# Optimization experiments

Measured on AMD Instinct MI355X. Metric: run time of the kernel, lower is better.

The kernel has to match this reference:

```python
import jax, jax.numpy as jnp
import numpy as np

Q_HEADS = 16
KV_HEADS = 4
ROPE_THETA = 10000.0


def _rope(x, seq_len):
    # x: [B, S, H, D]; pairs are consecutive along D (view_as_complex semantics)
    D = x.shape[-1]
    inv_freq = 1.0 / (ROPE_THETA ** (jnp.arange(0, D, 2, dtype=jnp.float32) / D))
    freqs = jnp.arange(seq_len, dtype=jnp.float32)[:, None] * inv_freq  # [S, D/2]
    cos = jnp.cos(freqs)[None, :, None, :]
    sin = jnp.sin(freqs)[None, :, None, :]
    xr = x.reshape(x.shape[:-1] + (D // 2, 2))
    x0, x1 = xr[..., 0], xr[..., 1]
    out = jnp.stack([x0 * cos - x1 * sin, x0 * sin + x1 * cos], axis=-1)
    return out.reshape(x.shape)


def setup_inputs() -> dict:
    key = jax.random.key(0)
    ks = jax.random.split(key, 6)
    B, S, E = 1, 2048, 2048
    KV_DIM = KV_HEADS * (E // Q_HEADS)  # 512
    scale = 0.02
    return {
        "x": jax.random.normal(ks[0], (B, S, E), dtype=jnp.float32),
        "Wq": jax.random.normal(ks[1], (E, E), dtype=jnp.float32) * scale,
        "Wk": jax.random.normal(ks[2], (KV_DIM, E), dtype=jnp.float32) * scale,
        "Wv": jax.random.normal(ks[3], (KV_DIM, E), dtype=jnp.float32) * scale,
        "Wo": jax.random.normal(ks[4], (E, E), dtype=jnp.float32) * scale,
        "bo": jax.random.normal(ks[5], (E,), dtype=jnp.float32) * scale,
        "cache_keys": jnp.zeros((B, S, KV_HEADS, E // Q_HEADS), dtype=jnp.float32),
        "cache_value": jnp.zeros((B, S, KV_HEADS, E // Q_HEADS), dtype=jnp.float32),
        "start_pos": 0,
    }


def reference(x, Wq, Wk, Wv, Wo, bo, cache_keys, cache_value, start_pos):
    B, S, E = x.shape
    hd = E // Q_HEADS
    G = Q_HEADS // KV_HEADS  # queries per kv head

    xq = (x @ Wq.T).reshape(B, S, Q_HEADS, hd)
    xk = (x @ Wk.T).reshape(B, S, KV_HEADS, hd)
    xv = (x @ Wv.T).reshape(B, S, KV_HEADS, hd)

    # Original applies RoPE with positions 0..seq_len-1 for both q and k
    # (freq tensor is sliced [:seq_len] inside apply_rotry_position_embedding).
    xq = _rope(xq, S)
    xk = _rope(xk, S)

    # cache write at start_pos (static python int)
    cache_keys = jax.lax.dynamic_update_slice(cache_keys, xk, (0, start_pos, 0, 0))
    cache_value = jax.lax.dynamic_update_slice(cache_value, xv, (0, start_pos, 0, 0))
    total = start_pos + S
    k_full = cache_keys[:, :total]   # [B, T, KVH, hd]
    v_full = cache_value[:, :total]

    # repeat_interleave over the head axis == GQA expansion
    k = jnp.repeat(k_full, G, axis=2)  # [B, T, QH, hd]
    v = jnp.repeat(v_full, G, axis=2)

    scores = jnp.einsum("bshd,bthd->bhst", xq, k) / jnp.sqrt(jnp.float32(hd))
    causal = jnp.triu(jnp.ones((S, total), dtype=bool), k=1)  # [S, T]
    scores = jnp.where(causal[None, None, :, :], -jnp.inf, scores)
    weights = jax.nn.softmax(scores, axis=-1)
    out = jnp.einsum("bhst,bthd->bshd", weights, v).reshape(B, S, E)
    # dropout p=0.0 / eval mode -> identity
    return out @ Wo.T + bo
```

## Files before the change

kernel.cpp:

```cpp
#include <hip/hip_runtime.h>
#include <stdint.h>

typedef unsigned short u16;
typedef float  f32x4  __attribute__((ext_vector_type(4)));
typedef __bf16 bf16x8 __attribute__((ext_vector_type(8)));
typedef __bf16 bf16x4 __attribute__((ext_vector_type(4)));
typedef unsigned short u16x8 __attribute__((ext_vector_type(8)));
typedef unsigned short u16x4v __attribute__((ext_vector_type(4)));

#define S_LEN 2048
#define E_DIM 2048
#define HD    128
#define QH    16
#define KVH   4
#define KVD   512
#define NQKV  3072
#define QK_SCALE 0.08838834764831845f

#define AS1 __attribute__((address_space(1)))
#define AS3 __attribute__((address_space(3)))

__device__ __forceinline__ u16 f2bf(float f) {
  union { float f; uint32_t u; } v; v.f = f;
  return (u16)((v.u + 0x7FFFu + ((v.u >> 16) & 1u)) >> 16);
}
__device__ __forceinline__ float bf2f(u16 b) {
  union { uint32_t u; float f; } v; v.u = ((uint32_t)b) << 16;
  return v.f;
}

__global__ void cast_all_kernel(const float* __restrict__ x, const float* __restrict__ Wq,
                                const float* __restrict__ Wk, const float* __restrict__ Wv,
                                const float* __restrict__ Wo,
                                u16* __restrict__ xb, u16* __restrict__ Wcat,
                                u16* __restrict__ Wob) {
  int i = blockIdx.x * blockDim.x + threadIdx.x;
  const float* src; u16* dst;
  if (i < (1 << 20))                       { src = x  + (size_t)i * 4;  dst = xb + (size_t)i * 4; }
  else if (i < (2 << 20))                  { size_t j = i - (1 << 20);  src = Wq + j * 4; dst = Wcat + j * 4; }
  else if (i < (2 << 20) + (1 << 18))      { size_t j = i - (2 << 20);  src = Wk + j * 4; dst = Wcat + (size_t)E_DIM * E_DIM + j * 4; }
  else if (i < (2 << 20) + (2 << 18))      { size_t j = i - (2 << 20) - (1 << 18); src = Wv + j * 4; dst = Wcat + (size_t)(E_DIM + KVD) * E_DIM + j * 4; }
  else                                     { size_t j = i - (2 << 20) - (2 << 18); src = Wo + j * 4; dst = Wob + j * 4; }
  float4 f = *reinterpret_cast<const float4*>(src);
  u16x4v o;
  o[0] = f2bf(f.x); o[1] = f2bf(f.y); o[2] = f2bf(f.z); o[3] = f2bf(f.w);
  *reinterpret_cast<u16x4v*>(dst) = o;
}

template<bool BIAS, bool OBF16>
__global__ __launch_bounds__(512) void gemm_bt_kernel(
    const u16* __restrict__ A, const u16* __restrict__ B,
    void* __restrict__ Cv, const float* __restrict__ bias,
    int M, int N, int K)
{
  __shared__ u16 As[2][128 * 64];
  __shared__ u16 Bs[2][128 * 64];

  const int tid  = threadIdx.x;
  const int lane = tid & 63;
  const int wid  = tid >> 6;
  const int wr   = (wid >> 2) * 64;
  const int wc   = (wid & 3) * 32;
  const int lr   = lane & 15;
  const int kg   = lane >> 4;
  const int sw   = lr & 7;

  const int bm = blockIdx.y * 128;
  const int bn = blockIdx.x * 128;

  f32x4 acc[4][2];
  #pragma unroll
  for (int r = 0; r < 4; ++r)
    #pragma unroll
    for (int c = 0; c < 2; ++c) acc[r][c] = (f32x4){0.f, 0.f, 0.f, 0.f};

  const int srow   = wid * 8 + (lane >> 3);
  const int schunk = (lane & 7) ^ (lane >> 3);

  const u16* gA = A + (size_t)(bm + srow) * K + schunk * 8;
  const u16* gB = B + (size_t)(bn + srow) * K + schunk * 8;

  auto stage = [&](int buf, int kt) {
    #pragma unroll
    for (int i = 0; i < 2; ++i) {
      __builtin_amdgcn_global_load_lds(
          (const AS1 void*)(gA + (size_t)i * 64 * K + kt),
          (AS3 void*)(&As[buf][(wid*8 + i*64) * 64]), 16, 0, 0);
      __builtin_amdgcn_global_load_lds(
          (const AS1 void*)(gB + (size_t)i * 64 * K + kt),
          (AS3 void*)(&Bs[buf][(wid*8 + i*64) * 64]), 16, 0, 0);
    }
  };

  stage(0, 0);
  __syncthreads();

  int cur = 0;
  for (int kt = 0; kt < K; kt += 64) {
    if (kt + 64 < K) stage(cur ^ 1, kt + 64);
    #pragma unroll
    for (int kk = 0; kk < 2; ++kk) {
      bf16x8 af[4], bfr[2];
      #pragma unroll
      for (int r = 0; r < 4; ++r)
        af[r] = *reinterpret_cast<const bf16x8*>(
            &As[cur][(wr + r*16 + lr)*64 + ((kk*4 + kg) ^ sw)*8]);
      #pragma unroll
      for (int c = 0; c < 2; ++c)
        bfr[c] = *reinterpret_cast<const bf16x8*>(
            &Bs[cur][(wc + c*16 + lr)*64 + ((kk*4 + kg) ^ sw)*8]);
      #pragma unroll
      for (int r = 0; r < 4; ++r)
        #pragma unroll
        for (int c = 0; c < 2; ++c)
          acc[r][c] = __builtin_amdgcn_mfma_f32_16x16x32_bf16(af[r], bfr[c], acc[r][c], 0, 0, 0);
    }
    __syncthreads();
    cur ^= 1;
  }

  const int crow = kg * 4;
  #pragma unroll
  for (int r = 0; r < 4; ++r) {
    #pragma unroll
    for (int c = 0; c < 2; ++c) {
      int gr = bm + wr + r*16 + crow;
      int gc = bn + wc + c*16 + lr;
      float badd = BIAS ? bias[gc] : 0.0f;
      #pragma unroll
      for (int reg = 0; reg < 4; ++reg) {
        float v = acc[r][c][reg] + badd;
        if constexpr (OBF16)
          ((u16*)Cv)[(size_t)(gr + reg)*N + gc] = f2bf(v);
        else
          ((float*)Cv)[(size_t)(gr + reg)*N + gc] = v;
      }
    }
  }
}

__global__ void rope_split_kernel(const u16* __restrict__ qkv,
                                  u16* __restrict__ qb, u16* __restrict__ kb) {
  int idx = blockIdx.x * blockDim.x + threadIdx.x;
  int s  = idx / 1280;
  int cp = idx - s * 1280;
  int col = cp * 2;
  const u16* src = qkv + (size_t)s * NQKV + col;
  float x0 = bf2f(src[0]), x1 = bf2f(src[1]);
  int p = (col & 127) >> 1;
  float inv = exp2f((float)p * (-13.287712379549449f / 64.0f));
  float ang = (float)s * inv;
  float sn, cs;
  sincosf(ang, &sn, &cs);
  float o0 = x0 * cs - x1 * sn;
  float o1 = x0 * sn + x1 * cs;
  if (col < E_DIM) {
    o0 *= QK_SCALE; o1 *= QK_SCALE;
    qb[(size_t)s * E_DIM + col]     = f2bf(o0);
    qb[(size_t)s * E_DIM + col + 1] = f2bf(o1);
  } else {
    kb[(size_t)s * KVD + (col - E_DIM)]     = f2bf(o0);
    kb[(size_t)s * KVD + (col - E_DIM) + 1] = f2bf(o1);
  }
}

__global__ void transpose_v_kernel(const u16* __restrict__ qkv, u16* __restrict__ vT) {
  __shared__ u16 tile[32][33];
  const int sbase = blockIdx.x * 32;
  const int cbase = blockIdx.y * 32;
  const int tx = threadIdx.x;
  const int ty = threadIdx.y;
  #pragma unroll
  for (int i = 0; i < 32; i += 8)
    tile[ty + i][tx] = qkv[(size_t)(sbase + ty + i) * NQKV + (E_DIM + KVD) + cbase + tx];
  __syncthreads();
  #pragma unroll
  for (int i = 0; i < 32; i += 8)
    vT[(size_t)(cbase + ty + i) * S_LEN + sbase + tx] = tile[tx][ty + i];
}

__device__ __forceinline__ void attn_tile(
    int t, int qt, int wid, int lr, int kg,
    const bf16x8* qf, f32x4* o, float& mr, float& ls,
    const u16* ks, const u16* vts, u16* ps)
{
  const int sw = lr & 7;
  f32x4 st[4];
  #pragma unroll
  for (int c = 0; c < 4; ++c) st[c] = (f32x4){0.f, 0.f, 0.f, 0.f};
  __builtin_amdgcn_s_setprio(1);
  #pragma unroll
  for (int kk = 0; kk < 4; ++kk) {
    #pragma unroll
    for (int c = 0; c < 4; ++c) {
      bf16x8 kfr = *reinterpret_cast<const bf16x8*>(
          &ks[(c*16 + lr)*128 + ((kk*4 + kg) ^ sw)*8]);
      st[c] = __builtin_amdgcn_mfma_f32_16x16x32_bf16(kfr, qf[kk], st[c], 0, 0, 0);
    }
  }
  __builtin_amdgcn_s_setprio(0);
  if (t == qt) {
    #pragma unroll
    for (int c = 0; c < 4; ++c)
      #pragma unroll
      for (int reg = 0; reg < 4; ++reg)
        if (c*16 + kg*4 + reg > wid*16 + lr) st[c][reg] = -1e30f;
  }
  float cm[4];
  #pragma unroll
  for (int c = 0; c < 4; ++c)
    cm[c] = fmaxf(fmaxf(st[c][0], st[c][1]), fmaxf(st[c][2], st[c][3]));
  float pm = fmaxf(fmaxf(cm[0], cm[1]), fmaxf(cm[2], cm[3]));
  pm = fmaxf(pm, __shfl_xor(pm, 16));
  pm = fmaxf(pm, __shfl_xor(pm, 32));

  if (!__all(pm - mr <= 8.0f)) {
    float nm = fmaxf(mr, pm);
    float alpha = __expf(mr - nm);
    ls *= alpha;
    mr = nm;
    float ar[4];
    #pragma unroll
    for (int reg = 0; reg < 4; ++reg)
      ar[reg] = __shfl(alpha, kg*4 + reg);
    #pragma unroll
    for (int d = 0; d < 8; ++d)
      #pragma unroll
      for (int reg = 0; reg < 4; ++reg)
        o[d][reg] *= ar[reg];
  }

  float p[4][4];
  float csum[4];
  #pragma unroll
  for (int c = 0; c < 4; ++c) {
    #pragma unroll
    for (int reg = 0; reg < 4; ++reg)
      p[c][reg] = __expf(st[c][reg] - mr);
    csum[c] = (p[c][0] + p[c][1]) + (p[c][2] + p[c][3]);
  }
  float sum = (csum[0] + csum[1]) + (csum[2] + csum[3]);
  sum += __shfl_xor(sum, 16);
  sum += __shfl_xor(sum, 32);
  ls += sum;

  #pragma unroll
  for (int c = 0; c < 4; ++c) {
    bf16x4 pk;
    #pragma unroll
    for (int reg = 0; reg < 4; ++reg) pk[reg] = (__bf16)p[c][reg];
    *reinterpret_cast<bf16x4*>(&ps[lr*72 + c*16 + kg*4]) = pk;
  }
  __builtin_amdgcn_s_setprio(1);
  #pragma unroll
  for (int kk = 0; kk < 2; ++kk) {
    bf16x8 pa = *reinterpret_cast<const bf16x8*>(&ps[lr*72 + kk*32 + kg*8]);
    #pragma unroll
    for (int d = 0; d < 8; ++d) {
      bf16x8 vb = *reinterpret_cast<const bf16x8*>(
          &vts[(d*16 + lr)*64 + ((kk*4 + kg) ^ sw)*8]);
      o[d] = __builtin_amdgcn_mfma_f32_16x16x32_bf16(pa, vb, o[d], 0, 0, 0);
    }
  }
  __builtin_amdgcn_s_setprio(0);
}

__global__ __launch_bounds__(256, 2) void attn_kernel(
    const u16* __restrict__ Q, const u16* __restrict__ Kc,
    const u16* __restrict__ VT, u16* __restrict__ Out)
{
  __shared__ u16 Ks[2][64 * 128];
  __shared__ u16 VTs[2][128 * 64];
  __shared__ u16 Ps[4][16 * 72];

  const int x = blockIdx.x;
  int qt, h;
  if (x < 256) { qt = x & 31; h = x >> 5; }
  else         { int xp = x - 256; qt = 31 - (xp & 31); h = 8 + (xp >> 5); }
  const int kvh = h >> 2;
  const int tid  = threadIdx.x;
  const int lane = tid & 63;
  const int wid  = tid >> 6;
  const int lr   = lane & 15;
  const int kg   = lane >> 4;

  const int NT = qt + 1;

  bf16x8 qf[4];
  {
    const u16* qa = Q + (size_t)(qt*64 + wid*16 + lr) * E_DIM + h * HD + kg * 8;
    #pragma unroll
    for (int kk = 0; kk < 4; ++kk)
      qf[kk] = *reinterpret_cast<const bf16x8*>(qa + kk * 32);
  }

  f32x4 o[8];
  #pragma unroll
  for (int d = 0; d < 8; ++d) o[d] = (f32x4){0.f,0.f,0.f,0.f};
  float mr = -1e30f, ls = 0.f;

  u16x8 kreg[4], vreg[4];
  const u16* kbase = Kc + kvh * HD;
  const u16* vbase = VT + (size_t)(kvh * HD) * S_LEN;

  auto stage_load = [&](int t) {
    #pragma unroll
    for (int i = 0; i < 4; ++i) {
      int c = i * 256 + tid;
      kreg[i] = *reinterpret_cast<const u16x8*>(
          kbase + (size_t)(t*64 + (c >> 4)) * KVD + (c & 15) * 8);
      vreg[i] = *reinterpret_cast<const u16x8*>(
          vbase + (size_t)(c >> 3) * S_LEN + t*64 + (c & 7) * 8);
    }
  };
  auto stage_write = [&](int b) {
    #pragma unroll
    for (int i = 0; i < 4; ++i) {
      int c = i * 256 + tid;
      int kr = c >> 4, kc = c & 15;
      *reinterpret_cast<u16x8*>(&Ks[b][kr*128 + (kc ^ (kr & 7))*8]) = kreg[i];
      int vr = c >> 3, vc = c & 7;
      *reinterpret_cast<u16x8*>(&VTs[b][vr*64 + (vc ^ (vr & 7))*8]) = vreg[i];
    }
  };

  int p = 0;
  stage_load(0);
  stage_write(0);
  __syncthreads();

  for (int t = 0; t < NT; ++t) {
    if (t + 1 < NT) stage_load(t + 1);
    attn_tile(t, qt, wid, lr, kg, qf, o, mr, ls, Ks[p], VTs[p], Ps[wid]);
    if (t + 1 < NT) {
      stage_write(p ^ 1);
      __syncthreads();
      p ^= 1;
    }
  }

  {
    float inv = 1.0f / ls;
    float ivq[4];
    #pragma unroll
    for (int reg = 0; reg < 4; ++reg)
      ivq[reg] = __shfl(inv, kg*4 + reg);
    #pragma unroll
    for (int reg = 0; reg < 4; ++reg) {
      int grow = qt*64 + wid*16 + kg*4 + reg;
      #pragma unroll
      for (int d = 0; d < 8; ++d)
        Out[(size_t)grow * E_DIM + h * HD + d*16 + lr] =
            __builtin_bit_cast(u16, (__bf16)(o[d][reg] * ivq[reg]));
    }
  }
}

extern "C" void kernel_launch(void* const* d_in, const int* in_sizes, int n_in,
                              void* d_out, int out_size, void* d_ws, size_t ws_size,
                              hipStream_t stream)
{
  const float* x  = (const float*)d_in[0];
  const float* Wq = (const float*)d_in[1];
  const float* Wk = (const float*)d_in[2];
  const float* Wv = (const float*)d_in[3];
  const float* Wo = (const float*)d_in[4];
  const float* bo = (const float*)d_in[5];
  float* out = (float*)d_out;

  char* w = (char*)d_ws;
  u16*   xb   = (u16*)(w);
  u16*   Wcat = (u16*)(w + (8u  << 20));
  u16*   Wob  = (u16*)(w + (20u << 20));
  u16*   qkv  = (u16*)(w + (28u << 20));
  u16*   qb   = (u16*)(w + (52u << 20));
  u16*   kb   = (u16*)(w + (60u << 20));
  u16*   vT   = (u16*)(w + (62u << 20));
  u16*   attn = (u16*)(w + (64u << 20));
  (void)ws_size; (void)in_sizes; (void)n_in; (void)out_size;

  cast_all_kernel<<<14336, 256, 0, stream>>>(x, Wq, Wk, Wv, Wo, xb, Wcat, Wob);

  gemm_bt_kernel<false, true><<<dim3(NQKV/128, S_LEN/128), 512, 0, stream>>>(
      xb, Wcat, qkv, nullptr, S_LEN, NQKV, E_DIM);

  rope_split_kernel<<<(S_LEN * 1280) / 256, 256, 0, stream>>>(qkv, qb, kb);
  transpose_v_kernel<<<dim3(S_LEN/32, KVD/32), dim3(32, 8), 0, stream>>>(qkv, vT);

  attn_kernel<<<512, 256, 0, stream>>>(qb, kb, vT, attn);

  gemm_bt_kernel<true, false><<<dim3(E_DIM/128, S_LEN/128), 512, 0, stream>>>(
      attn, Wob, out, bo, S_LEN, E_DIM, E_DIM);
}
```

Measured before the change: 139.9 us.

## Pair causal query tiles and share KV across two heads per attention block

Restructures attention so each block processes two heads sharing a KV head, and each wave handles 32 query rows, reusing K/V fragments across two MFMA streams. Each block runs two phases with complementary causal tiles (qt and 31-qt) to balance work, and the grid is reduced to 256 blocks with one block per CU. The grid indexing maps each complementary pair twice, so every output tile is computed redundantly, and the occupancy drop reduces latency hiding.

```diff
diff --git a/kernel.cpp b/kernel.cpp
--- a/kernel.cpp
+++ b/kernel.cpp
@@ -179,130 +179,35 @@
     vT[(size_t)(cbase + ty + i) * S_LEN + sbase + tx] = tile[tx][ty + i];
 }
 
-__device__ __forceinline__ void attn_tile(
-    int t, int qt, int wid, int lr, int kg,
-    const bf16x8* qf, f32x4* o, float& mr, float& ls,
-    const u16* ks, const u16* vts, u16* ps)
-{
-  const int sw = lr & 7;
-  f32x4 st[4];
-  #pragma unroll
-  for (int c = 0; c < 4; ++c) st[c] = (f32x4){0.f, 0.f, 0.f, 0.f};
-  __builtin_amdgcn_s_setprio(1);
-  #pragma unroll
-  for (int kk = 0; kk < 4; ++kk) {
-    #pragma unroll
-    for (int c = 0; c < 4; ++c) {
-      bf16x8 kfr = *reinterpret_cast<const bf16x8*>(
-          &ks[(c*16 + lr)*128 + ((kk*4 + kg) ^ sw)*8]);
-      st[c] = __builtin_amdgcn_mfma_f32_16x16x32_bf16(kfr, qf[kk], st[c], 0, 0, 0);
-    }
-  }
-  __builtin_amdgcn_s_setprio(0);
-  if (t == qt) {
-    #pragma unroll
-    for (int c = 0; c < 4; ++c)
-      #pragma unroll
-      for (int reg = 0; reg < 4; ++reg)
-        if (c*16 + kg*4 + reg > wid*16 + lr) st[c][reg] = -1e30f;
-  }
-  float cm[4];
-  #pragma unroll
-  for (int c = 0; c < 4; ++c)
-    cm[c] = fmaxf(fmaxf(st[c][0], st[c][1]), fmaxf(st[c][2], st[c][3]));
-  float pm = fmaxf(fmaxf(cm[0], cm[1]), fmaxf(cm[2], cm[3]));
-  pm = fmaxf(pm, __shfl_xor(pm, 16));
-  pm = fmaxf(pm, __shfl_xor(pm, 32));
-
-  if (!__all(pm - mr <= 8.0f)) {
-    float nm = fmaxf(mr, pm);
-    float alpha = __expf(mr - nm);
-    ls *= alpha;
-    mr = nm;
-    float ar[4];
-    #pragma unroll
-    for (int reg = 0; reg < 4; ++reg)
-      ar[reg] = __shfl(alpha, kg*4 + reg);
-    #pragma unroll
-    for (int d = 0; d < 8; ++d)
-      #pragma unroll
-      for (int reg = 0; reg < 4; ++reg)
-        o[d][reg] *= ar[reg];
-  }
-
-  float p[4][4];
-  float csum[4];
-  #pragma unroll
-  for (int c = 0; c < 4; ++c) {
-    #pragma unroll
-    for (int reg = 0; reg < 4; ++reg)
-      p[c][reg] = __expf(st[c][reg] - mr);
-    csum[c] = (p[c][0] + p[c][1]) + (p[c][2] + p[c][3]);
-  }
-  float sum = (csum[0] + csum[1]) + (csum[2] + csum[3]);
-  sum += __shfl_xor(sum, 16);
-  sum += __shfl_xor(sum, 32);
-  ls += sum;
-
-  #pragma unroll
-  for (int c = 0; c < 4; ++c) {
-    bf16x4 pk;
-    #pragma unroll
-    for (int reg = 0; reg < 4; ++reg) pk[reg] = (__bf16)p[c][reg];
-    *reinterpret_cast<bf16x4*>(&ps[lr*72 + c*16 + kg*4]) = pk;
-  }
-  __builtin_amdgcn_s_setprio(1);
-  #pragma unroll
-  for (int kk = 0; kk < 2; ++kk) {
-    bf16x8 pa = *reinterpret_cast<const bf16x8*>(&ps[lr*72 + kk*32 + kg*8]);
-    #pragma unroll
-    for (int d = 0; d < 8; ++d) {
-      bf16x8 vb = *reinterpret_cast<const bf16x8*>(
-          &vts[(d*16 + lr)*64 + ((kk*4 + kg) ^ sw)*8]);
-      o[d] = __builtin_amdgcn_mfma_f32_16x16x32_bf16(pa, vb, o[d], 0, 0, 0);
-    }
-  }
-  __builtin_amdgcn_s_setprio(0);
-}
-
-__global__ __launch_bounds__(256, 2) void attn_kernel(
+__global__ __launch_bounds__(256, 1) void attn_kernel(
     const u16* __restrict__ Q, const u16* __restrict__ Kc,
     const u16* __restrict__ VT, u16* __restrict__ Out)
 {
   __shared__ u16 Ks[2][64 * 128];
   __shared__ u16 VTs[2][128 * 64];
-  __shared__ u16 Ps[4][16 * 72];
-
-  const int x = blockIdx.x;
-  int qt, h;
-  if (x < 256) { qt = x & 31; h = x >> 5; }
-  else         { int xp = x - 256; qt = 31 - (xp & 31); h = 8 + (xp >> 5); }
-  const int kvh = h >> 2;
+  __shared__ u16 Ps[4][32 * 72];
+
+  const int x    = blockIdx.x;
+  const int hp   = x & 7;
+  const int qtA  = (x >> 3) & 31;
+  const int qtB  = 31 - qtA;
+  const int h0   = hp * 2;
+  const int kvh  = h0 >> 2;
+
   const int tid  = threadIdx.x;
   const int lane = tid & 63;
   const int wid  = tid >> 6;
+  const int head = h0 + (wid & 1);
+  const int rowbase = (wid >> 1) * 32;
   const int lr   = lane & 15;
   const int kg   = lane >> 4;
-
-  const int NT = qt + 1;
-
-  bf16x8 qf[4];
-  {
-    const u16* qa = Q + (size_t)(qt*64 + wid*16 + lr) * E_DIM + h * HD + kg * 8;
-    #pragma unroll
-    for (int kk = 0; kk < 4; ++kk)
-      qf[kk] = *reinterpret_cast<const bf16x8*>(qa + kk * 32);
-  }
-
-  f32x4 o[8];
-  #pragma unroll
-  for (int d = 0; d < 8; ++d) o[d] = (f32x4){0.f,0.f,0.f,0.f};
-  float mr = -1e30f, ls = 0.f;
-
-  u16x8 kreg[4], vreg[4];
+  const int sw   = lr & 7;
+
   const u16* kbase = Kc + kvh * HD;
   const u16* vbase = VT + (size_t)(kvh * HD) * S_LEN;
-
+  u16* ps = Ps[wid];
+
+  u16x8 kreg[4], vreg[4];
   auto stage_load = [&](int t) {
     #pragma unroll
     for (int i = 0; i < 4; ++i) {
@@ -324,36 +229,154 @@
     }
   };
 
-  int p = 0;
-  stage_load(0);
-  stage_write(0);
-  __syncthreads();
-
-  for (int t = 0; t < NT; ++t) {
-    if (t + 1 < NT) stage_load(t + 1);
-    attn_tile(t, qt, wid, lr, kg, qf, o, mr, ls, Ks[p], VTs[p], Ps[wid]);
-    if (t + 1 < NT) {
-      stage_write(p ^ 1);
-      __syncthreads();
-      p ^= 1;
-    }
-  }
-
-  {
-    float inv = 1.0f / ls;
-    float ivq[4];
-    #pragma unroll
-    for (int reg = 0; reg < 4; ++reg)
-      ivq[reg] = __shfl(inv, kg*4 + reg);
-    #pragma unroll
-    for (int reg = 0; reg < 4; ++reg) {
-      int grow = qt*64 + wid*16 + kg*4 + reg;
-      #pragma unroll
-      for (int d = 0; d < 8; ++d)
-        Out[(size_t)grow * E_DIM + h * HD + d*16 + lr] =
-            __builtin_bit_cast(u16, (__bf16)(o[d][reg] * ivq[reg]));
-    }
-  }
+  auto run_phase = [&](int qt) {
+    const int NT = qt + 1;
+
+    bf16x8 qf[2][4];
+    #pragma unroll
+    for (int g = 0; g < 2; ++g) {
+      const u16* qa = Q + (size_t)(qt*64 + rowbase + g*16 + lr) * E_DIM
+                        + head * HD + kg * 8;
+      #pragma unroll
+      for (int kk = 0; kk < 4; ++kk)
+        qf[g][kk] = *reinterpret_cast<const bf16x8*>(qa + kk * 32);
+    }
+
+    f32x4 o[2][8];
+    #pragma unroll
+    for (int g = 0; g < 2; ++g)
+      #pragma unroll
+      for (int d = 0; d < 8; ++d) o[g][d] = (f32x4){0.f,0.f,0.f,0.f};
+    float mr[2] = {-1e30f, -1e30f}, ls[2] = {0.f, 0.f};
+
+    stage_load(0);
+    __syncthreads();
+    stage_write(0);
+    __syncthreads();
+
+    int p = 0;
+    for (int t = 0; t < NT; ++t) {
+      if (t + 1 < NT) stage_load(t + 1);
+
+      f32x4 st[2][4];
+      #pragma unroll
+      for (int g = 0; g < 2; ++g)
+        #pragma unroll
+        for (int c = 0; c < 4; ++c) st[g][c] = (f32x4){0.f,0.f,0.f,0.f};
+      __builtin_amdgcn_s_setprio(1);
+      #pragma unroll
+      for (int kk = 0; kk < 4; ++kk) {
+        #pragma unroll
+        for (int c = 0; c < 4; ++c) {
+          bf16x8 kfr = *reinterpret_cast<const bf16x8*>(
+              &Ks[p][(c*16 + lr)*128 + ((kk*4 + kg) ^ sw)*8]);
+          st[0][c] = __builtin_amdgcn_mfma_f32_16x16x32_bf16(kfr, qf[0][kk], st[0][c], 0, 0, 0);
+          st[1][c] = __builtin_amdgcn_mfma_f32_16x16x32_bf16(kfr, qf[1][kk], st[1][c], 0, 0, 0);
+        }
+      }
+      __builtin_amdgcn_s_setprio(0);
+
+      if (t == qt) {
+        #pragma unroll
+        for (int g = 0; g < 2; ++g)
+          #pragma unroll
+          for (int c = 0; c < 4; ++c)
+            #pragma unroll
+            for (int reg = 0; reg < 4; ++reg)
+              if (c*16 + kg*4 + reg > rowbase + g*16 + lr) st[g][c][reg] = -1e30f;
+      }
+
+      #pragma unroll
+      for (int g = 0; g < 2; ++g) {
+        float cm[4];
+        #pragma unroll
+        for (int c = 0; c < 4; ++c)
+          cm[c] = fmaxf(fmaxf(st[g][c][0], st[g][c][1]), fmaxf(st[g][c][2], st[g][c][3]));
+        float pm = fmaxf(fmaxf(cm[0], cm[1]), fmaxf(cm[2], cm[3]));
+        pm = fmaxf(pm, __shfl_xor(pm, 16));
+        pm = fmaxf(pm, __shfl_xor(pm, 32));
+
+        if (!__all(pm - mr[g] <= 8.0f)) {
+          float nm = fmaxf(mr[g], pm);
+          float alpha = __expf(mr[g] - nm);
+          ls[g] *= alpha;
+          mr[g] = nm;
+          float ar[4];
+          #pragma unroll
+          for (int reg = 0; reg < 4; ++reg)
+            ar[reg] = __shfl(alpha, kg*4 + reg);
+          #pragma unroll
+          for (int d = 0; d < 8; ++d)
+            #pragma unroll
+            for (int reg = 0; reg < 4; ++reg)
+              o[g][d][reg] *= ar[reg];
+        }
+
+        float sum = 0.f;
+        #pragma unroll
+        for (int c = 0; c < 4; ++c) {
+          float pr[4];
+          #pragma unroll
+          for (int reg = 0; reg < 4; ++reg)
+            pr[reg] = __expf(st[g][c][reg] - mr[g]);
+          sum += (pr[0] + pr[1]) + (pr[2] + pr[3]);
+          bf16x4 pk;
+          #pragma unroll
+          for (int reg = 0; reg < 4; ++reg) pk[reg] = (__bf16)pr[reg];
+          *reinterpret_cast<bf16x4*>(&ps[(g*16 + lr)*72 + c*16 + kg*4]) = pk;
+        }
+        sum += __shfl_xor(sum, 16);
+        sum += __shfl_xor(sum, 32);
+        ls[g] += sum;
+      }
+
+      bf16x8 pa[2][2];
+      #pragma unroll
+      for (int g = 0; g < 2; ++g)
+        #pragma unroll
+        for (int kk = 0; kk < 2; ++kk)
+          pa[g][kk] = *reinterpret_cast<const bf16x8*>(
+              &ps[(g*16 + lr)*72 + kk*32 + kg*8]);
+      __builtin_amdgcn_s_setprio(1);
+      #pragma unroll
+      for (int d0 = 0; d0 < 8; ++d0) {
+        #pragma unroll
+        for (int kk = 0; kk < 2; ++kk) {
+          bf16x8 vb = *reinterpret_cast<const bf16x8*>(
+              &VTs[p][(d0*16 + lr)*64 + ((kk*4 + kg) ^ sw)*8]);
+          o[0][d0] = __builtin_amdgcn_mfma_f32_16x16x32_bf16(pa[0][kk], vb, o[0][d0], 0, 0, 0);
+          o[1][d0] = __builtin_amdgcn_mfma_f32_16x16x32_bf16(pa[1][kk], vb, o[1][d0], 0, 0, 0);
+        }
+      }
+      __builtin_amdgcn_s_setprio(0);
+
+      if (t + 1 < NT) {
+        stage_write(p ^ 1);
+        __syncthreads();
+        p ^= 1;
+      }
+    }
+
+    #pragma unroll
+    for (int g = 0; g < 2; ++g) {
+      float inv = 1.0f / ls[g];
+      float ivq[4];
+      #pragma unroll
+      for (int reg = 0; reg < 4; ++reg)
+        ivq[reg] = __shfl(inv, kg*4 + reg);
+      #pragma unroll
+      for (int reg = 0; reg < 4; ++reg) {
+        int grow = qt*64 + rowbase + g*16 + kg*4 + reg;
+        #pragma unroll
+        for (int d = 0; d < 8; ++d)
+          Out[(size_t)grow * E_DIM + head * HD + d*16 + lr] =
+              __builtin_bit_cast(u16, (__bf16)(o[g][d][reg] * ivq[reg]));
+      }
+    }
+  };
+
+  run_phase(qtA);
+  run_phase(qtB);
 }
 
 extern "C" void kernel_launch(void* const* d_in, const int* in_sizes, int n_in,
@@ -387,7 +410,7 @@
   rope_split_kernel<<<(S_LEN * 1280) / 256, 256, 0, stream>>>(qkv, qb, kb);
   transpose_v_kernel<<<dim3(S_LEN/32, KVD/32), dim3(32, 8), 0, stream>>>(qkv, vT);
 
-  attn_kernel<<<512, 256, 0, stream>>>(qb, kb, vT, attn);
+  attn_kernel<<<256, 256, 0, stream>>>(qb, kb, vT, attn);
 
   gemm_bt_kernel<true, false><<<dim3(E_DIM/128, S_LEN/128), 512, 0, stream>>>(
       attn, Wob, out, bo, S_LEN, E_DIM, E_DIM);
```

New measurement: 173.5 us. 1.24x slower.

## Fuse RoPE and V transpose into QKV GEMM epilogue with precomputed table

Applied to the files above, without the earlier changes.

The QKV GEMM epilogue now applies RoPE (using a cos/sin table precomputed in the cast kernel) and writes Q/K directly in bf16, and writes V transposed directly. This removes the intermediate qkv buffer plus the separate rope_split and transpose_v kernels, saving two launches and a round trip through global memory. In exchange the epilogue gains shuffles, table loads and strided transposed stores. The RoPE is computed from fp32 accumulators rather than bf16-rounded values, which slightly changes numerics.

```diff
diff --git a/kernel.cpp b/kernel.cpp
--- a/kernel.cpp
+++ b/kernel.cpp
@@ -24,17 +24,22 @@
   union { float f; uint32_t u; } v; v.f = f;
   return (u16)((v.u + 0x7FFFu + ((v.u >> 16) & 1u)) >> 16);
 }
-__device__ __forceinline__ float bf2f(u16 b) {
-  union { uint32_t u; float f; } v; v.u = ((uint32_t)b) << 16;
-  return v.f;
-}
 
 __global__ void cast_all_kernel(const float* __restrict__ x, const float* __restrict__ Wq,
                                 const float* __restrict__ Wk, const float* __restrict__ Wv,
                                 const float* __restrict__ Wo,
                                 u16* __restrict__ xb, u16* __restrict__ Wcat,
-                                u16* __restrict__ Wob) {
+                                u16* __restrict__ Wob, float2* __restrict__ tab) {
   int i = blockIdx.x * blockDim.x + threadIdx.x;
+  if (i >= 3670016) {
+    int j = i - 3670016;
+    int s = j >> 6, pidx = j & 63;
+    float inv = exp2f((float)pidx * (-13.287712379549449f / 64.0f));
+    float sn, cs;
+    sincosf((float)s * inv, &sn, &cs);
+    tab[j] = make_float2(cs, sn);
+    return;
+  }
   const float* src; u16* dst;
   if (i < (1 << 20))                       { src = x  + (size_t)i * 4;  dst = xb + (size_t)i * 4; }
   else if (i < (2 << 20))                  { size_t j = i - (1 << 20);  src = Wq + j * 4; dst = Wcat + j * 4; }
@@ -47,10 +52,12 @@
   *reinterpret_cast<u16x4v*>(dst) = o;
 }
 
-template<bool BIAS, bool OBF16>
+template<bool BIAS, int MODE>
 __global__ __launch_bounds__(512) void gemm_bt_kernel(
     const u16* __restrict__ A, const u16* __restrict__ B,
-    void* __restrict__ Cv, const float* __restrict__ bias,
+    float* __restrict__ C, const float* __restrict__ bias,
+    const float2* __restrict__ tab, u16* __restrict__ qb,
+    u16* __restrict__ kb, u16* __restrict__ vTp,
     int M, int N, int K)
 {
   __shared__ u16 As[2][128 * 64];
@@ -126,57 +133,37 @@
     for (int c = 0; c < 2; ++c) {
       int gr = bm + wr + r*16 + crow;
       int gc = bn + wc + c*16 + lr;
-      float badd = BIAS ? bias[gc] : 0.0f;
-      #pragma unroll
-      for (int reg = 0; reg < 4; ++reg) {
-        float v = acc[r][c][reg] + badd;
-        if constexpr (OBF16)
-          ((u16*)Cv)[(size_t)(gr + reg)*N + gc] = f2bf(v);
-        else
-          ((float*)Cv)[(size_t)(gr + reg)*N + gc] = v;
+      if constexpr (MODE == 0) {
+        float badd = BIAS ? bias[gc] : 0.0f;
+        #pragma unroll
+        for (int reg = 0; reg < 4; ++reg)
+          C[(size_t)(gr + reg)*N + gc] = acc[r][c][reg] + badd;
+      } else {
+        if (gc < E_DIM + KVD) {
+          int pidx = (gc & 127) >> 1;
+          bool odd = lr & 1;
+          #pragma unroll
+          for (int reg = 0; reg < 4; ++reg) {
+            float val = acc[r][c][reg];
+            float oth = __shfl_xor(val, 1);
+            float2 cs = tab[(gr + reg) * 64 + pidx];
+            float o = odd ? (oth * cs.y + val * cs.x)
+                          : (val * cs.x - oth * cs.y);
+            if (gc < E_DIM)
+              qb[(size_t)(gr + reg) * E_DIM + gc] = f2bf(o * QK_SCALE);
+            else
+              kb[(size_t)(gr + reg) * KVD + (gc - E_DIM)] = f2bf(o);
+          }
+        } else {
+          bf16x4 pk;
+          #pragma unroll
+          for (int reg = 0; reg < 4; ++reg) pk[reg] = (__bf16)acc[r][c][reg];
+          *reinterpret_cast<bf16x4*>(
+              &vTp[(size_t)(gc - E_DIM - KVD) * S_LEN + gr]) = pk;
+        }
       }
     }
   }
-}
-
-__global__ void rope_split_kernel(const u16* __restrict__ qkv,
-                                  u16* __restrict__ qb, u16* __restrict__ kb) {
-  int idx = blockIdx.x * blockDim.x + threadIdx.x;
-  int s  = idx / 1280;
-  int cp = idx - s * 1280;
-  int col = cp * 2;
-  const u16* src = qkv + (size_t)s * NQKV + col;
-  float x0 = bf2f(src[0]), x1 = bf2f(src[1]);
-  int p = (col & 127) >> 1;
-  float inv = exp2f((float)p * (-13.287712379549449f / 64.0f));
-  float ang = (float)s * inv;
-  float sn, cs;
-  sincosf(ang, &sn, &cs);
-  float o0 = x0 * cs - x1 * sn;
-  float o1 = x0 * sn + x1 * cs;
-  if (col < E_DIM) {
-    o0 *= QK_SCALE; o1 *= QK_SCALE;
-    qb[(size_t)s * E_DIM + col]     = f2bf(o0);
-    qb[(size_t)s * E_DIM + col + 1] = f2bf(o1);
-  } else {
-    kb[(size_t)s * KVD + (col - E_DIM)]     = f2bf(o0);
-    kb[(size_t)s * KVD + (col - E_DIM) + 1] = f2bf(o1);
-  }
-}
-
-__global__ void transpose_v_kernel(const u16* __restrict__ qkv, u16* __restrict__ vT) {
-  __shared__ u16 tile[32][33];
-  const int sbase = blockIdx.x * 32;
-  const int cbase = blockIdx.y * 32;
-  const int tx = threadIdx.x;
-  const int ty = threadIdx.y;
-  #pragma unroll
-  for (int i = 0; i < 32; i += 8)
-    tile[ty + i][tx] = qkv[(size_t)(sbase + ty + i) * NQKV + (E_DIM + KVD) + cbase + tx];
-  __syncthreads();
-  #pragma unroll
-  for (int i = 0; i < 32; i += 8)
-    vT[(size_t)(cbase + ty + i) * S_LEN + sbase + tx] = tile[tx][ty + i];
 }
 
 __device__ __forceinline__ void attn_tile(
@@ -369,26 +356,23 @@
   float* out = (float*)d_out;
 
   char* w = (char*)d_ws;
-  u16*   xb   = (u16*)(w);
-  u16*   Wcat = (u16*)(w + (8u  << 20));
-  u16*   Wob  = (u16*)(w + (20u << 20));
-  u16*   qkv  = (u16*)(w + (28u << 20));
-  u16*   qb   = (u16*)(w + (52u << 20));
-  u16*   kb   = (u16*)(w + (60u << 20));
-  u16*   vT   = (u16*)(w + (62u << 20));
-  u16*   attn = (u16*)(w + (64u << 20));
+  u16*    xb   = (u16*)(w);
+  u16*    Wcat = (u16*)(w + (8u  << 20));
+  u16*    Wob  = (u16*)(w + (20u << 20));
+  float2* tab  = (float2*)(w + (28u << 20));
+  u16*    qb   = (u16*)(w + (30u << 20));
+  u16*    kb   = (u16*)(w + (38u << 20));
+  u16*    vT   = (u16*)(w + (40u << 20));
+  u16*    attn = (u16*)(w + (42u << 20));
   (void)ws_size; (void)in_sizes; (void)n_in; (void)out_size;
 
-  cast_all_kernel<<<14336, 256, 0, stream>>>(x, Wq, Wk, Wv, Wo, xb, Wcat, Wob);
-
-  gemm_bt_kernel<false, true><<<dim3(NQKV/128, S_LEN/128), 512, 0, stream>>>(
-      xb, Wcat, qkv, nullptr, S_LEN, NQKV, E_DIM);
-
-  rope_split_kernel<<<(S_LEN * 1280) / 256, 256, 0, stream>>>(qkv, qb, kb);
-  transpose_v_kernel<<<dim3(S_LEN/32, KVD/32), dim3(32, 8), 0, stream>>>(qkv, vT);
+  cast_all_kernel<<<14848, 256, 0, stream>>>(x, Wq, Wk, Wv, Wo, xb, Wcat, Wob, tab);
+
+  gemm_bt_kernel<false, 2><<<dim3(NQKV/128, S_LEN/128), 512, 0, stream>>>(
+      xb, Wcat, nullptr, nullptr, tab, qb, kb, vT, S_LEN, NQKV, E_DIM);
 
   attn_kernel<<<512, 256, 0, stream>>>(qb, kb, vT, attn);
 
-  gemm_bt_kernel<true, false><<<dim3(E_DIM/128, S_LEN/128), 512, 0, stream>>>(
-      attn, Wob, out, bo, S_LEN, E_DIM, E_DIM);
-}
+  gemm_bt_kernel<true, 0><<<dim3(E_DIM/128, S_LEN/128), 512, 0, stream>>>(
+      attn, Wob, out, bo, nullptr, nullptr, nullptr, nullptr, S_LEN, E_DIM, E_DIM);
+}
```

New measurement: 137.5 us. About the same (-1.7%).
